# Kernel tuning notes

Measured on AMD Instinct MI355X. Metric: run time of the kernel, lower is better.

The kernel has to match this reference:

```python
import jax, jax.numpy as jnp
import numpy as np

IN_DIM = 1024
OUT_DIM = 1024
HIDDEN = 1024
T = 16384
R_MIN, R_MAX, MAX_PHASE = 0.9, 0.999, 6.28


@jax.vmap
def binary_operator_diag(q_i, q_j):
    A_i, b_i = q_i
    A_j, b_j = q_j
    return (A_j * A_i, A_j * b_i + b_j)


def setup_inputs() -> dict:
    key = jax.random.key(0)
    ks = jax.random.split(key, 8)
    inputs = jax.random.normal(ks[0], (T, IN_DIM), dtype=jnp.float32)
    # nu_log / theta_log per original initializers
    u1 = jax.random.uniform(ks[1], (HIDDEN,), dtype=jnp.float32)
    nu_log = jnp.log(-0.5 * jnp.log(u1 * (R_MAX ** 2 - R_MIN ** 2) + R_MIN ** 2))
    u2 = jax.random.uniform(ks[2], (HIDDEN,), dtype=jnp.float32)
    theta_log = jnp.log(MAX_PHASE * u2)
    diag_lambda = jnp.exp(-jnp.exp(nu_log) + 1j * jnp.exp(theta_log))
    gamma_log = jnp.log(jnp.sqrt(1 - jnp.abs(diag_lambda) ** 2))
    B_re = jax.random.normal(ks[3], (IN_DIM, HIDDEN), dtype=jnp.float32) / jnp.sqrt(2.0 * IN_DIM)
    B_im = jax.random.normal(ks[4], (IN_DIM, HIDDEN), dtype=jnp.float32) / jnp.sqrt(2.0 * IN_DIM)
    C_re = jax.random.normal(ks[5], (OUT_DIM, HIDDEN), dtype=jnp.float32) / jnp.sqrt(1.0 * HIDDEN)
    C_im = jax.random.normal(ks[6], (OUT_DIM, HIDDEN), dtype=jnp.float32) / jnp.sqrt(1.0 * HIDDEN)
    D = jax.random.normal(ks[7], (OUT_DIM, IN_DIM), dtype=jnp.float32)
    return {"inputs": inputs, "nu_log": nu_log, "theta_log": theta_log,
            "gamma_log": gamma_log, "B_re": B_re, "B_im": B_im,
            "C_re": C_re, "C_im": C_im, "D": D}


def reference(inputs, nu_log, theta_log, gamma_log, B_re, B_im, C_re, C_im, D):
    # diagonal complex transition eigenvalues, shape (H,)
    diag_lambda = jnp.exp(-jnp.exp(nu_log) + 1j * jnp.exp(theta_log))
    # NOTE: original code expands gamma on axis=-1 -> (H, 1); broadcasts against
    # B_norm (in_dim, H) because in_dim == hidden_dim. Reproduced faithfully.
    B_norm = (B_re + 1j * B_im) * jnp.exp(gamma_log)[:, None]
    C = C_re + 1j * C_im
    T_len = inputs.shape[-2]
    Lambda_elements = jnp.repeat(diag_lambda[None, :], T_len, axis=0)  # (T, H)
    Bu_elements = jnp.einsum('ih,ti->th', B_norm, inputs)              # (T, H) complex
    _, hidden_states = jax.lax.associative_scan(
        binary_operator_diag, (Lambda_elements, Bu_elements))
    outputs = jnp.real(jnp.einsum('th,oh->to', hidden_states, C))      # (T, out)
    outputs = outputs + jnp.einsum('ti,io->to', inputs, D)             # D used as 'io'
    return outputs
```

## Files before the change

kernel.cpp:

```cpp
#include <hip/hip_runtime.h>
#include <hip/hip_bf16.h>
#include <stdint.h>

#define T_LEN   16384
#define HID     1024
#define KDIM    1024
#define CHUNK   64
#define NCHUNK  256

typedef __bf16 bf16x8 __attribute__((ext_vector_type(8)));
typedef float  f32x4  __attribute__((ext_vector_type(4)));

__device__ inline ushort f2bf(float f) {
  union { float f; uint32_t u; } v; v.f = f;
  uint32_t r = v.u + 0x7FFF + ((v.u >> 16) & 1);
  return (ushort)(r >> 16);
}
__device__ inline float bf2f(ushort u) {
  union { uint32_t u; float f; } v; v.u = ((uint32_t)u) << 16;
  return v.f;
}

__device__ inline void gload16(const void* g, void* l) {
  __builtin_amdgcn_global_load_lds(
      (const __attribute__((address_space(1))) void*)g,
      (__attribute__((address_space(3))) void*)l, 16, 0, 0);
}

__global__ __launch_bounds__(256) void prep_kernel(
    const float* __restrict__ nu_log, const float* __restrict__ theta_log,
    const float* __restrict__ gamma_log,
    float* __restrict__ lam_re, float* __restrict__ lam_im, float* __restrict__ eg) {
  int h = blockIdx.x * 256 + threadIdx.x;
  if (h < HID) {
    float mag = expf(-expf(nu_log[h]));
    float th  = expf(theta_log[h]);
    lam_re[h] = mag * cosf(th);
    lam_im[h] = mag * sinf(th);
    eg[h]     = expf(gamma_log[h]);
  }
}

__global__ __launch_bounds__(256) void convX(
    const float* __restrict__ src, ushort* __restrict__ dst) {
  size_t i = ((size_t)blockIdx.x * 256 + threadIdx.x) * 4;
  float4 v = *(const float4*)(src + i);
  ushort4 o;
  o.x = f2bf(v.x); o.y = f2bf(v.y); o.z = f2bf(v.z); o.w = f2bf(v.w);
  *(ushort4*)(dst + i) = o;
}

__global__ __launch_bounds__(256) void weight_prep(
    const float* __restrict__ Bre, const float* __restrict__ Bim,
    const float* __restrict__ Cre, const float* __restrict__ Cim,
    const float* __restrict__ D,   const float* __restrict__ eg,
    ushort* __restrict__ BreT, ushort* __restrict__ BimT,
    ushort* __restrict__ CreB, ushort* __restrict__ CimB,
    ushort* __restrict__ DT) {
  __shared__ float tile[32][33];
  int z = blockIdx.z;
  if (z == 2 || z == 3) {
    const float* src = (z == 2) ? Cre : Cim;
    ushort* dst = (z == 2) ? CreB : CimB;
    float s = (z == 2) ? 1.0f : -1.0f;
    size_t base = ((size_t)blockIdx.y * 32 + (threadIdx.x >> 3)) * 1024 +
                  blockIdx.x * 32 + (threadIdx.x & 7) * 4;
    float4 v = *(const float4*)(src + base);
    ushort4 o;
    o.x = f2bf(v.x * s); o.y = f2bf(v.y * s);
    o.z = f2bf(v.z * s); o.w = f2bf(v.w * s);
    *(ushort4*)(dst + base) = o;
    return;
  }
  const float* src = (z == 0) ? Bre : (z == 1) ? Bim : D;
  ushort* dst = (z == 0) ? BreT : (z == 1) ? BimT : DT;
  bool scaled = (z < 2);
  int bx = blockIdx.x * 32;
  int by = blockIdx.y * 32;
  int tx = threadIdx.x & 31, ty = threadIdx.x >> 5;
#pragma unroll
  for (int r = 0; r < 32; r += 8)
    tile[ty + r][tx] = src[(size_t)(by + ty + r) * 1024 + bx + tx];
  __syncthreads();
  float sc = scaled ? eg[by + tx] : 1.0f;
#pragma unroll
  for (int r = 0; r < 32; r += 8)
    dst[(size_t)(bx + ty + r) * 1024 + by + tx] = f2bf(tile[tx][ty + r] * sc);
}


#define BAR()   __builtin_amdgcn_s_barrier()
#define SCH0()  __builtin_amdgcn_sched_barrier(0)
#define LGKM0() asm volatile("s_waitcnt lgkmcnt(0)")
#define VM4()   asm volatile("s_waitcnt vmcnt(4)")
#define VM0()   asm volatile("s_waitcnt vmcnt(0)")

#define STAGE_HALF(G, LDA, R0, K0, LT, HALF)                         \
  do {                                                               \
    _Pragma("unroll")                                                \
    for (int is_ = 0; is_ < 2; ++is_) {                              \
      int seg_ = w * 2 + is_;                                        \
      int gr_ = (R0) + (HALF) * 128 + seg_ * 8 + (l >> 3);           \
      int gc_ = (K0) + (((l & 7) ^ (l >> 3)) << 3);                  \
      gload16((G) + (size_t)gr_ * (LDA) + gc_,                       \
              (LT) + (HALF) * 8192 + seg_ * 512);                    \
    }                                                                \
  } while (0)

#define DS_A(QM, BUF)                                                \
  do {                                                               \
    _Pragma("unroll")                                                \
    for (int m_ = 0; m_ < 4; ++m_) {                                 \
      int r_ = (wr * 128 + ((QM) * 4 + m_) * 16 + lo) * 64;          \
      a[m_][0] = *(const bf16x8*)((BUF) + r_ + c0us);                \
      a[m_][1] = *(const bf16x8*)((BUF) + r_ + c1us);                \
    }                                                                \
  } while (0)

#define DS_B(QN, BUF, REG)                                           \
  do {                                                               \
    _Pragma("unroll")                                                \
    for (int n_ = 0; n_ < 2; ++n_) {                                 \
      int r_ = (wc * 64 + ((QN) * 2 + n_) * 16 + lo) * 64;           \
      REG[n_][0] = *(const bf16x8*)((BUF) + r_ + c0us);              \
      REG[n_][1] = *(const bf16x8*)((BUF) + r_ + c1us);              \
    }                                                                \
  } while (0)

#define MFMA_Q(QM, QN, REG)                                          \
  do {                                                               \
    __builtin_amdgcn_s_setprio(1);                                   \
    _Pragma("unroll")                                                \
    for (int m_ = 0; m_ < 4; ++m_)                                   \
      _Pragma("unroll")                                              \
      for (int n_ = 0; n_ < 2; ++n_) {                               \
        f32x4* ac_ = &acc[(QM) * 4 + m_][(QN) * 2 + n_];             \
        *ac_ = __builtin_amdgcn_mfma_f32_16x16x32_bf16(              \
            a[m_][0], REG[n_][0], *ac_, 0, 0, 0);                    \
        *ac_ = __builtin_amdgcn_mfma_f32_16x16x32_bf16(              \
            a[m_][1], REG[n_][1], *ac_, 0, 0, 0);                    \
      }                                                              \
    __builtin_amdgcn_s_setprio(0);                                   \
  } while (0)

__device__ __forceinline__ void gemm256_seg(
    const ushort* __restrict__ A, int lda, const ushort* __restrict__ B,
    ushort* lds, int row0, int col0,
    int w, int l, int wr, int wc, int lo, int q, int c0us, int c1us,
    f32x4 acc[8][4]) {
  ushort* A0 = lds;
  ushort* A1 = lds + 16384;
  ushort* B0 = lds + 32768;
  ushort* B1 = lds + 49152;
  bf16x8 a[4][2], bq0[2][2], bq1[2][2];
  STAGE_HALF(A, lda, row0, 0, A0, 0);
  STAGE_HALF(A, lda, row0, 0, A0, 1);
  STAGE_HALF(B, 1024, col0, 0, B0, 0);
  STAGE_HALF(B, 1024, col0, 0, B0, 1);
  STAGE_HALF(B, 1024, col0, 64, B1, 0);
  STAGE_HALF(B, 1024, col0, 64, B1, 1);
  VM4(); BAR();
  for (int i = 0; i < 8; ++i) {
    const int k1 = (2 * i + 1) * 64;
    const int k2 = (2 * i + 2) * 64;
    const int k3 = (2 * i + 3) * 64;
    const bool st2 = (i < 7);
    DS_A(0, A0); DS_B(0, B0, bq0);
    STAGE_HALF(A, lda, row0, k1, A1, 0);
    BAR(); LGKM0(); SCH0(); MFMA_Q(0, 0, bq0); BAR();
    DS_B(1, B0, bq1);
    STAGE_HALF(A, lda, row0, k1, A1, 1);
    BAR(); LGKM0(); SCH0(); MFMA_Q(0, 1, bq1); BAR();
    DS_A(1, A0);
    if (st2) STAGE_HALF(B, 1024, col0, k2, B0, 0);
    BAR(); LGKM0(); SCH0(); MFMA_Q(1, 0, bq0); BAR();
    if (st2) { STAGE_HALF(B, 1024, col0, k2, B0, 1); VM4(); } else { VM0(); }
    BAR(); LGKM0(); SCH0(); MFMA_Q(1, 1, bq1); BAR();
    DS_A(0, A1); DS_B(0, B1, bq0);
    if (st2) STAGE_HALF(A, lda, row0, k2, A0, 0);
    BAR(); LGKM0(); SCH0(); MFMA_Q(0, 0, bq0); BAR();
    DS_B(1, B1, bq1);
    if (st2) STAGE_HALF(A, lda, row0, k2, A0, 1);
    BAR(); LGKM0(); SCH0(); MFMA_Q(0, 1, bq1); BAR();
    DS_A(1, A1);
    if (st2) STAGE_HALF(B, 1024, col0, k3, B1, 0);
    BAR(); LGKM0(); SCH0(); MFMA_Q(1, 0, bq0); BAR();
    if (st2) { STAGE_HALF(B, 1024, col0, k3, B1, 1); VM4(); } else { VM0(); }
    BAR(); LGKM0(); SCH0(); MFMA_Q(1, 1, bq1); BAR();
  }
}

__global__ __launch_bounds__(512, 2) void gemm_bu(
    const ushort* __restrict__ A, const ushort* __restrict__ B,
    ushort* __restrict__ O) {
  __shared__ __align__(16) ushort lds[65536];
  const int tid = threadIdx.x;
  const int w = tid >> 6, l = tid & 63;
  const int wr = w >> 2, wc = w & 3;
  const int lo = l & 15, q = l >> 4;
  const int xorv = (lo & 7) << 4;
  const int c0us = ((q * 16) ^ xorv) >> 1;
  const int c1us = ((64 + q * 16) ^ xorv) >> 1;
  const int id = blockIdx.x;
  const int xcd = id & 7, slot = id >> 3;
  const int row0 = (xcd * 8 + (slot >> 3)) * 256;
  const int col0 = (slot & 7) * 256;
  f32x4 acc[8][4];
#pragma unroll
  for (int m = 0; m < 8; ++m)
#pragma unroll
    for (int n = 0; n < 4; ++n) acc[m][n] = (f32x4){0.f, 0.f, 0.f, 0.f};
  gemm256_seg(A, 1024, B, lds, row0, col0, w, l, wr, wc, lo, q, c0us, c1us, acc);
  const int rowb = row0 + wr * 128, colb = col0 + wc * 64;
#pragma unroll
  for (int m = 0; m < 8; ++m)
#pragma unroll
    for (int n = 0; n < 4; ++n) {
      int col = colb + n * 16 + lo;
#pragma unroll
      for (int r = 0; r < 4; ++r)
        O[(size_t)(rowb + m * 16 + q * 4 + r) * 2048 + col] = f2bf(acc[m][n][r]);
    }
}

__global__ __launch_bounds__(512, 2) void gemm3(
    const ushort* __restrict__ Hall,
    const ushort* __restrict__ CreB, const ushort* __restrict__ CimB,
    const ushort* __restrict__ X,    const ushort* __restrict__ DT,
    float* __restrict__ O) {
  __shared__ __align__(16) ushort lds[65536];
  const int tid = threadIdx.x;
  const int w = tid >> 6, l = tid & 63;
  const int wr = w >> 2, wc = w & 3;
  const int lo = l & 15, q = l >> 4;
  const int xorv = (lo & 7) << 4;
  const int c0us = ((q * 16) ^ xorv) >> 1;
  const int c1us = ((64 + q * 16) ^ xorv) >> 1;
  const int id = blockIdx.x;
  const int xcd = id & 7, slot = id >> 3;
  const int row0 = (xcd * 8 + (slot >> 2)) * 256;
  const int col0 = (slot & 3) * 256;
  f32x4 acc[8][4];
#pragma unroll
  for (int m = 0; m < 8; ++m)
#pragma unroll
    for (int n = 0; n < 4; ++n) acc[m][n] = (f32x4){0.f, 0.f, 0.f, 0.f};
  gemm256_seg(Hall,        2048, CreB, lds, row0, col0, w, l, wr, wc, lo, q, c0us, c1us, acc);
  gemm256_seg(Hall + 1024, 2048, CimB, lds, row0, col0, w, l, wr, wc, lo, q, c0us, c1us, acc);
  gemm256_seg(X,           1024, DT,   lds, row0, col0, w, l, wr, wc, lo, q, c0us, c1us, acc);
  const int rowb = row0 + wr * 128, colb = col0 + wc * 64;
#pragma unroll
  for (int m = 0; m < 8; ++m)
#pragma unroll
    for (int n = 0; n < 4; ++n) {
      int col = colb + n * 16 + lo;
#pragma unroll
      for (int r = 0; r < 4; ++r)
        O[(size_t)(rowb + m * 16 + q * 4 + r) * HID + col] = acc[m][n][r];
    }
}

__global__ __launch_bounds__(256) void scan_sums(
    const ushort* __restrict__ Bu,
    const float* __restrict__ lam_re, const float* __restrict__ lam_im,
    float* __restrict__ Sre, float* __restrict__ Sim) {
  int h0 = (blockIdx.y * 256 + threadIdx.x) * 2;
  int c = blockIdx.x;
  float lr0 = lam_re[h0], li0 = lam_im[h0];
  float lr1 = lam_re[h0 + 1], li1 = lam_im[h0 + 1];
  float hr0 = 0.f, hi0 = 0.f, hr1 = 0.f, hi1 = 0.f;
  const uint* P = (const uint*)Bu;
  size_t baseR = (size_t)c * CHUNK * 1024 + (h0 >> 1);
  size_t baseI = baseR + 512;
#pragma unroll 8
  for (int t = 0; t < CHUNK; ++t) {
    uint re = P[baseR + (size_t)t * 1024];
    uint im = P[baseI + (size_t)t * 1024];
    float br0 = bf2f((ushort)re), br1 = bf2f((ushort)(re >> 16));
    float bi0 = bf2f((ushort)im), bi1 = bf2f((ushort)(im >> 16));
    float nr0 = fmaf(lr0, hr0, fmaf(-li0, hi0, br0));
    float ni0 = fmaf(lr0, hi0, fmaf(li0, hr0, bi0));
    float nr1 = fmaf(lr1, hr1, fmaf(-li1, hi1, br1));
    float ni1 = fmaf(lr1, hi1, fmaf(li1, hr1, bi1));
    hr0 = nr0; hi0 = ni0; hr1 = nr1; hi1 = ni1;
  }
  Sre[(size_t)c * HID + h0] = hr0;  Sre[(size_t)c * HID + h0 + 1] = hr1;
  Sim[(size_t)c * HID + h0] = hi0;  Sim[(size_t)c * HID + h0 + 1] = hi1;
}

__global__ __launch_bounds__(256) void scan_carry(
    const float* __restrict__ Sre, const float* __restrict__ Sim,
    const float* __restrict__ lam_re, const float* __restrict__ lam_im,
    float* __restrict__ Pre, float* __restrict__ Pim) {
  int h = blockIdx.x * 256 + threadIdx.x;
  float lr = lam_re[h], li = lam_im[h];
  float pr = lr, pi = li;
#pragma unroll
  for (int s = 0; s < 6; ++s) {
    float nr = pr * pr - pi * pi;
    float ni = 2.f * pr * pi;
    pr = nr; pi = ni;
  }
  float cr = 0.f, ci = 0.f;
  for (int c = 0; c < NCHUNK; ++c) {
    Pre[(size_t)c * HID + h] = cr;
    Pim[(size_t)c * HID + h] = ci;
    float sr = Sre[(size_t)c * HID + h];
    float si = Sim[(size_t)c * HID + h];
    float nr = fmaf(pr, cr, fmaf(-pi, ci, sr));
    float ni = fmaf(pr, ci, fmaf(pi, cr, si));
    cr = nr; ci = ni;
  }
}

__global__ __launch_bounds__(256) void scan_emit(
    const ushort* __restrict__ Bu,
    const float* __restrict__ lam_re, const float* __restrict__ lam_im,
    const float* __restrict__ Pre, const float* __restrict__ Pim,
    ushort* __restrict__ Hall) {
  int h0 = (blockIdx.y * 256 + threadIdx.x) * 2;
  int c = blockIdx.x;
  float lr0 = lam_re[h0], li0 = lam_im[h0];
  float lr1 = lam_re[h0 + 1], li1 = lam_im[h0 + 1];
  float hr0 = Pre[(size_t)c * HID + h0], hi0 = Pim[(size_t)c * HID + h0];
  float hr1 = Pre[(size_t)c * HID + h0 + 1], hi1 = Pim[(size_t)c * HID + h0 + 1];
  const uint* P = (const uint*)Bu;
  uint* Q = (uint*)Hall;
  size_t baseR = (size_t)c * CHUNK * 1024 + (h0 >> 1);
  size_t baseI = baseR + 512;
#pragma unroll 8
  for (int t = 0; t < CHUNK; ++t) {
    uint re = P[baseR + (size_t)t * 1024];
    uint im = P[baseI + (size_t)t * 1024];
    float br0 = bf2f((ushort)re), br1 = bf2f((ushort)(re >> 16));
    float bi0 = bf2f((ushort)im), bi1 = bf2f((ushort)(im >> 16));
    float nr0 = fmaf(lr0, hr0, fmaf(-li0, hi0, br0));
    float ni0 = fmaf(lr0, hi0, fmaf(li0, hr0, bi0));
    float nr1 = fmaf(lr1, hr1, fmaf(-li1, hi1, br1));
    float ni1 = fmaf(lr1, hi1, fmaf(li1, hr1, bi1));
    hr0 = nr0; hi0 = ni0; hr1 = nr1; hi1 = ni1;
    Q[baseR + (size_t)t * 1024] = (uint)f2bf(hr0) | ((uint)f2bf(hr1) << 16);
    Q[baseI + (size_t)t * 1024] = (uint)f2bf(hi0) | ((uint)f2bf(hi1) << 16);
  }
}

extern "C" void kernel_launch(void* const* d_in, const int* in_sizes, int n_in,
                              void* d_out, int out_size, void* d_ws, size_t ws_size,
                              hipStream_t stream) {
  const float* inputs    = (const float*)d_in[0];
  const float* nu_log    = (const float*)d_in[1];
  const float* theta_log = (const float*)d_in[2];
  const float* gamma_log = (const float*)d_in[3];
  const float* B_re      = (const float*)d_in[4];
  const float* B_im      = (const float*)d_in[5];
  const float* C_re      = (const float*)d_in[6];
  const float* C_im      = (const float*)d_in[7];
  const float* D         = (const float*)d_in[8];
  float* out = (float*)d_out;

  char* ws = (char*)d_ws;
  constexpr size_t TH = (size_t)T_LEN * HID;
  constexpr size_t W  = (size_t)1024 * 1024;
  constexpr size_t CH = (size_t)NCHUNK * HID;

  ushort* Xbf  = (ushort*)(ws);
  ushort* Bu   = (ushort*)(ws + TH * 2);
  ushort* Hall = (ushort*)(ws + TH * 6);
  char*   p    = ws + TH * 10;
  ushort* Ball = (ushort*)(p);             p += 2 * W * 2;
  ushort* CreB = (ushort*)(p);             p += W * 2;
  ushort* CimB = (ushort*)(p);             p += W * 2;
  ushort* DT   = (ushort*)(p);             p += W * 2;
  float*  Sre  = (float*)(p);              p += CH * 4;
  float*  Sim  = (float*)(p);              p += CH * 4;
  float*  Pre  = (float*)(p);              p += CH * 4;
  float*  Pim  = (float*)(p);              p += CH * 4;
  float*  lamR = (float*)(p);              p += 4096;
  float*  lamI = (float*)(p);              p += 4096;
  float*  eg   = (float*)(p);              p += 4096;
  ushort* BreT = Ball;
  ushort* BimT = Ball + W;

  prep_kernel<<<dim3(HID / 256), 256, 0, stream>>>(nu_log, theta_log, gamma_log,
                                                   lamR, lamI, eg);
  convX<<<dim3((unsigned)(TH / 4 / 256)), 256, 0, stream>>>(inputs, Xbf);
  weight_prep<<<dim3(32, 32, 5), 256, 0, stream>>>(B_re, B_im, C_re, C_im, D, eg,
                                                   BreT, BimT, CreB, CimB, DT);

  gemm_bu<<<dim3(512), 512, 0, stream>>>(Xbf, Ball, Bu);

  scan_sums<<<dim3(NCHUNK, HID / 512), 256, 0, stream>>>(Bu, lamR, lamI, Sre, Sim);
  scan_carry<<<dim3(HID / 256), 256, 0, stream>>>(Sre, Sim, lamR, lamI, Pre, Pim);
  scan_emit<<<dim3(NCHUNK, HID / 512), 256, 0, stream>>>(Bu, lamR, lamI, Pre, Pim,
                                                         Hall);

  gemm3<<<dim3(256), 512, 0, stream>>>(Hall, CreB, CimB, Xbf, DT, out);
}
```

Measured before the change: 354.5 us.

## Halve GEMM barriers and merge three K-segments into one continuous pipeline

Replaces the two-barrier-per-quarter GEMM main loop with a single compiler-fenced barrier per MFMA quarter. It drops the explicit lgkmcnt(0) waits and sched_barriers and leaves LDS-read ordering to the compiler. The three back-to-back GEMM segments in gemm3 become one 48-tile pipeline, so the prologue and drain happen once instead of three times, and the main loop is no longer unrolled. A-tile staging is now issued as one call instead of being split across two quarters. This risks LDS write-after-read hazards and weaker control over MFMA/load interleaving.

After: 340.9 us. 1.04x faster.

```diff
diff --git a/kernel.cpp b/kernel.cpp
--- a/kernel.cpp
+++ b/kernel.cpp
@@ -90,10 +90,10 @@
 
 
 #define BAR()   __builtin_amdgcn_s_barrier()
-#define SCH0()  __builtin_amdgcn_sched_barrier(0)
-#define LGKM0() asm volatile("s_waitcnt lgkmcnt(0)")
-#define VM4()   asm volatile("s_waitcnt vmcnt(4)")
-#define VM0()   asm volatile("s_waitcnt vmcnt(0)")
+#define FEN()   asm volatile("" ::: "memory")
+#define VM4()   asm volatile("s_waitcnt vmcnt(4)" ::: "memory")
+#define VM0()   asm volatile("s_waitcnt vmcnt(0)" ::: "memory")
+#define PBAR()  do { FEN(); BAR(); FEN(); } while (0)
 
 #define STAGE_HALF(G, LDA, R0, K0, LT, HALF)                         \
   do {                                                               \
@@ -143,50 +143,71 @@
     __builtin_amdgcn_s_setprio(0);                                   \
   } while (0)
 
-__device__ __forceinline__ void gemm256_seg(
-    const ushort* __restrict__ A, int lda, const ushort* __restrict__ B,
+template<int NSEG>
+__device__ __forceinline__ void gemm256_1bar(
+    const ushort* Ap0, int ld0, const ushort* Bp0,
+    const ushort* Ap1, int ld1, const ushort* Bp1,
+    const ushort* Ap2, int ld2, const ushort* Bp2,
     ushort* lds, int row0, int col0,
-    int w, int l, int wr, int wc, int lo, int q, int c0us, int c1us,
-    f32x4 acc[8][4]) {
+    int w, int l, int wr, int wc, int lo, int c0us, int c1us,
+    f32x4 (&acc)[8][4]) {
   ushort* A0 = lds;
   ushort* A1 = lds + 16384;
   ushort* B0 = lds + 32768;
   ushort* B1 = lds + 49152;
   bf16x8 a[4][2], bq0[2][2], bq1[2][2];
-  STAGE_HALF(A, lda, row0, 0, A0, 0);
-  STAGE_HALF(A, lda, row0, 0, A0, 1);
-  STAGE_HALF(B, 1024, col0, 0, B0, 0);
-  STAGE_HALF(B, 1024, col0, 0, B0, 1);
-  STAGE_HALF(B, 1024, col0, 64, B1, 0);
-  STAGE_HALF(B, 1024, col0, 64, B1, 1);
-  VM4(); BAR();
-  for (int i = 0; i < 8; ++i) {
-    const int k1 = (2 * i + 1) * 64;
-    const int k2 = (2 * i + 2) * 64;
-    const int k3 = (2 * i + 3) * 64;
-    const bool st2 = (i < 7);
+  const int NT = NSEG * 16;
+
+  auto stageA = [&](int t, ushort* buf) {
+    const ushort* A; int lda;
+    if constexpr (NSEG == 1) { A = Ap0; lda = ld0; }
+    else {
+      if (t < 16)      { A = Ap0; lda = ld0; }
+      else if (t < 32) { A = Ap1; lda = ld1; }
+      else             { A = Ap2; lda = ld2; }
+    }
+    const int kk = (t & 15) * 64;
+    STAGE_HALF(A, lda, row0, kk, buf, 0);
+    STAGE_HALF(A, lda, row0, kk, buf, 1);
+  };
+  auto stageB = [&](int t, ushort* buf) {
+    const ushort* B;
+    if constexpr (NSEG == 1) { B = Bp0; }
+    else {
+      if (t < 16)      B = Bp0;
+      else if (t < 32) B = Bp1;
+      else             B = Bp2;
+    }
+    const int kk = (t & 15) * 64;
+    STAGE_HALF(B, 1024, col0, kk, buf, 0);
+    STAGE_HALF(B, 1024, col0, kk, buf, 1);
+  };
+
+  stageA(0, A0); stageB(0, B0); stageB(1, B1);
+  VM4(); PBAR();
+
+#pragma unroll 1
+  for (int j = 0; j < NT / 2; ++j) {
+    const int t1 = 2 * j + 1, t2 = 2 * j + 2, t3 = 2 * j + 3;
+    const bool st = (t2 < NT);
     DS_A(0, A0); DS_B(0, B0, bq0);
-    STAGE_HALF(A, lda, row0, k1, A1, 0);
-    BAR(); LGKM0(); SCH0(); MFMA_Q(0, 0, bq0); BAR();
+    stageA(t1, A1);
+    PBAR(); MFMA_Q(0, 0, bq0);
     DS_B(1, B0, bq1);
-    STAGE_HALF(A, lda, row0, k1, A1, 1);
-    BAR(); LGKM0(); SCH0(); MFMA_Q(0, 1, bq1); BAR();
+    PBAR(); MFMA_Q(0, 1, bq1);
     DS_A(1, A0);
-    if (st2) STAGE_HALF(B, 1024, col0, k2, B0, 0);
-    BAR(); LGKM0(); SCH0(); MFMA_Q(1, 0, bq0); BAR();
-    if (st2) { STAGE_HALF(B, 1024, col0, k2, B0, 1); VM4(); } else { VM0(); }
-    BAR(); LGKM0(); SCH0(); MFMA_Q(1, 1, bq1); BAR();
+    PBAR(); MFMA_Q(1, 0, bq0);
+    if (st) { stageB(t2, B0); VM4(); } else { VM0(); }
+    PBAR(); MFMA_Q(1, 1, bq1);
     DS_A(0, A1); DS_B(0, B1, bq0);
-    if (st2) STAGE_HALF(A, lda, row0, k2, A0, 0);
-    BAR(); LGKM0(); SCH0(); MFMA_Q(0, 0, bq0); BAR();
+    if (st) stageA(t2, A0);
+    PBAR(); MFMA_Q(0, 0, bq0);
     DS_B(1, B1, bq1);
-    if (st2) STAGE_HALF(A, lda, row0, k2, A0, 1);
-    BAR(); LGKM0(); SCH0(); MFMA_Q(0, 1, bq1); BAR();
+    PBAR(); MFMA_Q(0, 1, bq1);
     DS_A(1, A1);
-    if (st2) STAGE_HALF(B, 1024, col0, k3, B1, 0);
-    BAR(); LGKM0(); SCH0(); MFMA_Q(1, 0, bq0); BAR();
-    if (st2) { STAGE_HALF(B, 1024, col0, k3, B1, 1); VM4(); } else { VM0(); }
-    BAR(); LGKM0(); SCH0(); MFMA_Q(1, 1, bq1); BAR();
+    PBAR(); MFMA_Q(1, 0, bq0);
+    if (st) { stageB(t3, B1); VM4(); }
+    PBAR(); MFMA_Q(1, 1, bq1);
   }
 }
 
@@ -210,7 +231,8 @@
   for (int m = 0; m < 8; ++m)
 #pragma unroll
     for (int n = 0; n < 4; ++n) acc[m][n] = (f32x4){0.f, 0.f, 0.f, 0.f};
-  gemm256_seg(A, 1024, B, lds, row0, col0, w, l, wr, wc, lo, q, c0us, c1us, acc);
+  gemm256_1bar<1>(A, 1024, B, A, 1024, B, A, 1024, B,
+                  lds, row0, col0, w, l, wr, wc, lo, c0us, c1us, acc);
   const int rowb = row0 + wr * 128, colb = col0 + wc * 64;
 #pragma unroll
   for (int m = 0; m < 8; ++m)
@@ -245,9 +267,10 @@
   for (int m = 0; m < 8; ++m)
 #pragma unroll
     for (int n = 0; n < 4; ++n) acc[m][n] = (f32x4){0.f, 0.f, 0.f, 0.f};
-  gemm256_seg(Hall,        2048, CreB, lds, row0, col0, w, l, wr, wc, lo, q, c0us, c1us, acc);
-  gemm256_seg(Hall + 1024, 2048, CimB, lds, row0, col0, w, l, wr, wc, lo, q, c0us, c1us, acc);
-  gemm256_seg(X,           1024, DT,   lds, row0, col0, w, l, wr, wc, lo, q, c0us, c1us, acc);
+  gemm256_1bar<3>(Hall, 2048, CreB,
+                  Hall + 1024, 2048, CimB,
+                  X, 1024, DT,
+                  lds, row0, col0, w, l, wr, wc, lo, c0us, c1us, acc);
   const int rowb = row0 + wr * 128, colb = col0 + wc * 64;
 #pragma unroll
   for (int m = 0; m < 8; ++m)
```
